# Optimization experiments

Measured on AMD Instinct MI355X. Metric: run time of the kernel, lower is better.

The kernel has to match this reference:

```python
import jax, jax.numpy as jnp
import numpy as np

B, C, D, H, W = 2, 256, 16, 16, 16
R, G = 8, 4  # low rank r=min(8,C//4)=8, groups g=min(4,C)=4
N = D * H * W


def setup_inputs() -> dict:
    key = jax.random.key(0)
    ks = jax.random.split(key, 16)
    s = 0.05  # weight scale keeps softmax logits in a sane range
    inp = {
        'fL': jax.random.normal(ks[0], (B, C, D, H, W), jnp.float32),
        'fU': jax.random.normal(ks[1], (B, C, D, H, W), jnp.float32),
        'qL_w': jax.random.normal(ks[2], (R, C), jnp.float32) * s,
        'qL_b': jnp.zeros((R,), jnp.float32),
        'kU_w': jax.random.normal(ks[3], (R, C), jnp.float32) * s,
        'kU_b': jnp.zeros((R,), jnp.float32),
        'vU_w': jax.random.normal(ks[4], (G, C // G, C // G), jnp.float32) * s,
        'vU_b': jnp.zeros((C,), jnp.float32),
        'qU_w': jax.random.normal(ks[5], (R, C), jnp.float32) * s,
        'qU_b': jnp.zeros((R,), jnp.float32),
        'kL_w': jax.random.normal(ks[6], (R, C), jnp.float32) * s,
        'kL_b': jnp.zeros((R,), jnp.float32),
        'vL_w': jax.random.normal(ks[7], (G, C // G, C // G), jnp.float32) * s,
        'vL_b': jnp.zeros((C,), jnp.float32),
        'beta': jnp.float32(0.5),
    }
    return inp


def _conv1x1(x, w, b):
    # x: [B, C, N]; w: [O, C] (1x1x1 conv == per-voxel linear)
    return jnp.einsum('oc,bcn->bon', w, x) + b[None, :, None]


def _gconv1x1(x, w, b):
    # grouped 1x1x1 conv; x: [B, C, N]; w: [G, Cg_out, Cg_in]
    xg = x.reshape(B, G, C // G, N)
    yg = jnp.einsum('goi,bgin->bgon', w, xg)
    return yg.reshape(B, C, N) + b[None, :, None]


def _attend(q, k, v):
    # q,k: [B, R, N]; v: [B, C, N]
    attn = jax.nn.softmax(jnp.einsum('brn,brm->bnm', q, k), axis=-1)  # [B,N,N]
    return jnp.einsum('bcn,bnm->bcm', v, attn)  # bmm(v, attn)


def reference(fL, fU, qL_w, qL_b, kU_w, kU_b, vU_w, vU_b,
              qU_w, qU_b, kL_w, kL_b, vL_w, vL_b, beta):
    xL = fL.reshape(B, C, N)
    xU = fU.reshape(B, C, N)
    LU = _attend(_conv1x1(xL, qL_w, qL_b), _conv1x1(xU, kU_w, kU_b),
                 _gconv1x1(xU, vU_w, vU_b))
    UL = _attend(_conv1x1(xU, qU_w, qU_b), _conv1x1(xL, kL_w, kL_b),
                 _gconv1x1(xL, vL_w, vL_b))
    fL2 = fL + beta * LU.reshape(B, C, D, H, W)
    fU2 = fU + beta * UL.reshape(B, C, D, H, W)
    return (fL2, fU2)
```

## Files before the change

kernel.cpp:

```cpp
#include <hip/hip_runtime.h>
#include <hip/hip_bf16.h>

#define B_  2
#define C_  256
#define N_  4096
#define R_  8
#define G_  4
#define CG_ 64

typedef __attribute__((ext_vector_type(8))) short short8;
typedef __attribute__((ext_vector_type(4))) float f32x4;

#define MFMA16(a, b, c) __builtin_amdgcn_mfma_f32_16x16x32_bf16((a), (b), (c), 0, 0, 0)
#define EXP2F(x) __builtin_amdgcn_exp2f(x)
#define LOG2E 1.44269504088896f

__device__ inline unsigned int pk2(float a, float b) {
    union { __hip_bfloat162 h; unsigned int u; } cv;
    cv.h = __float22bfloat162_rn(float2{a, b});
    return cv.u;
}
__device__ inline unsigned short f2bf(float f) {
    union { __hip_bfloat16 h; unsigned short u; } cv;
    cv.h = __float2bfloat16(f);
    return cv.u;
}

#define QF_OFF   0
#define KF_OFF   524288
#define VF_OFF   1048576
#define L2Z_OFFF 2621440

#define XS2 264

__global__ __launch_bounds__(256) void fused_pre(
    const float* __restrict__ fL, const float* __restrict__ fU,
    const float* __restrict__ qLw, const float* __restrict__ qLb,
    const float* __restrict__ kLw, const float* __restrict__ kLb,
    const float* __restrict__ vLw, const float* __restrict__ vLb,
    const float* __restrict__ qUw, const float* __restrict__ qUb,
    const float* __restrict__ kUw, const float* __restrict__ kUb,
    const float* __restrict__ vUw, const float* __restrict__ vUb,
    unsigned short* __restrict__ wsu)
{
    const int s   = blockIdx.z >> 1;
    const int b   = blockIdx.z & 1;
    const int nc0 = blockIdx.x;
    const int n0  = nc0 * 32;
    const int t   = threadIdx.x;

    const float* x  = (s ? fU : fL) + (size_t)b * C_ * N_;
    const float* wq = s ? qUw : qLw;
    const float* bq = s ? qUb : qLb;
    const float* wk = s ? kUw : kLw;
    const float* bk = s ? kUb : kLb;
    const float* wv = s ? vUw : vLw;
    const float* bv = s ? vUb : vLb;
    const int dq = s, dk = 1 - s, dv = 1 - s;

    __shared__ __align__(16) unsigned short xs[32 * XS2];
    __shared__ __align__(16) unsigned short vtmp[256 * 48];
    __shared__ __align__(16) float qtmp[2][16][17];

    {
        const int cp = t >> 1;
        const int nh = (t & 1) * 16;
        const float* r0 = x + (size_t)(2 * cp) * N_ + n0 + nh;
        const float* r1 = r0 + N_;
        float4 a[4], bb[4];
#pragma unroll
        for (int j = 0; j < 4; j++) {
            a[j]  = *reinterpret_cast<const float4*>(r0 + j * 4);
            bb[j] = *reinterpret_cast<const float4*>(r1 + j * 4);
        }
        unsigned int* xd = reinterpret_cast<unsigned int*>(xs);
#pragma unroll
        for (int j = 0; j < 4; j++) {
            xd[(nh + j * 4 + 0) * (XS2 / 2) + cp] = pk2(a[j].x, bb[j].x);
            xd[(nh + j * 4 + 1) * (XS2 / 2) + cp] = pk2(a[j].y, bb[j].y);
            xd[(nh + j * 4 + 2) * (XS2 / 2) + cp] = pk2(a[j].z, bb[j].z);
            xd[(nh + j * 4 + 3) * (XS2 / 2) + cp] = pk2(a[j].w, bb[j].w);
        }
    }
    __syncthreads();

    const int w  = t >> 6;
    const int l  = t & 63;
    const int lm = l & 15;
    const int q  = l >> 4;
    const int ncl = w & 1;
    const int gh  = w >> 1;

    short8 bf[8];
    const unsigned short* xrow = xs + (ncl * 16 + lm) * XS2 + q * 8;
    if (gh == 0) {
#pragma unroll
        for (int kc = 0; kc < 8; kc++)
            bf[kc] = *reinterpret_cast<const short8*>(xrow + kc * 32);
    } else {
#pragma unroll
        for (int kc = 4; kc < 8; kc++)
            bf[kc] = *reinterpret_cast<const short8*>(xrow + kc * 32);
    }

    if (gh == 0) {
        const int o = lm;
        const float* wrow = (o < 8) ? (wq + o * C_) : (wk + (o - 8) * C_);
        const float scl = (o < 8) ? LOG2E : 1.0f;
        f32x4 pa = {0.f, 0.f, 0.f, 0.f};
#pragma unroll
        for (int kc = 0; kc < 8; kc++) {
            const float4 w0 = *reinterpret_cast<const float4*>(wrow + kc * 32 + q * 8);
            const float4 w1 = *reinterpret_cast<const float4*>(wrow + kc * 32 + q * 8 + 4);
            union { unsigned int u[4]; short8 v; } aw;
            aw.u[0] = pk2(w0.x * scl, w0.y * scl);
            aw.u[1] = pk2(w0.z * scl, w0.w * scl);
            aw.u[2] = pk2(w1.x * scl, w1.y * scl);
            aw.u[3] = pk2(w1.z * scl, w1.w * scl);
            pa = MFMA16(aw.v, bf[kc], pa);
        }
#pragma unroll
        for (int r = 0; r < 4; r++) {
            const int oo = q * 4 + r;
            const float v = pa[r] + ((q < 2) ? bq[oo] * LOG2E : bk[oo - 8]);
            qtmp[w][oo][lm] = v;
        }
        const int nt = nc0 * 2 + w;
        uint4 pq = {0u, 0u, 0u, 0u}, pk = {0u, 0u, 0u, 0u};
        if (q == 0) {
            float aq[8], ak[8];
#pragma unroll
            for (int o2 = 0; o2 < 8; o2++) { aq[o2] = qtmp[w][o2][lm]; ak[o2] = qtmp[w][8 + o2][lm]; }
            pq.x = pk2(aq[0], aq[1]); pq.y = pk2(aq[2], aq[3]);
            pq.z = pk2(aq[4], aq[5]); pq.w = pk2(aq[6], aq[7]);
            pk.x = pk2(ak[0], ak[1]); pk.y = pk2(ak[2], ak[3]);
            pk.z = pk2(ak[4], ak[5]); pk.w = pk2(ak[6], ak[7]);
        }
        *reinterpret_cast<uint4*>(wsu + QF_OFF + ((size_t)(dq * B_ + b) * 256 + nt) * 512 + l * 8) = pq;
        *reinterpret_cast<uint4*>(wsu + KF_OFF + ((size_t)(dk * B_ + b) * 256 + nt) * 512 + l * 8) = pk;
    }

    {
#pragma unroll
        for (int gi = 0; gi < 2; gi++) {
            const int g = gh * 2 + gi;
#pragma unroll
            for (int ocb = 0; ocb < 4; ocb++) {
                f32x4 ca = {0.f, 0.f, 0.f, 0.f};
#pragma unroll
                for (int kc2 = 0; kc2 < 2; kc2++) {
                    const float* wr = wv + (size_t)g * (CG_ * CG_)
                                    + (ocb * 16 + lm) * CG_ + kc2 * 32 + q * 8;
                    const float4 w0 = *reinterpret_cast<const float4*>(wr);
                    const float4 w1 = *reinterpret_cast<const float4*>(wr + 4);
                    union { unsigned int u[4]; short8 v; } aw;
                    aw.u[0] = pk2(w0.x, w0.y); aw.u[1] = pk2(w0.z, w0.w);
                    aw.u[2] = pk2(w1.x, w1.y); aw.u[3] = pk2(w1.z, w1.w);
                    ca = MFMA16(aw.v, bf[g * 2 + kc2], ca);
                }
#pragma unroll
                for (int r = 0; r < 4; r++) {
                    const int c = g * 64 + ocb * 16 + q * 4 + r;
                    vtmp[c * 48 + ncl * 16 + lm] = f2bf(ca[r] + bv[c]);
                }
            }
        }
    }
    __syncthreads();

    {
        const int db = dv * B_ + b;
#pragma unroll
        for (int ctl = 0; ctl < 4; ctl++) {
            const int ct = w * 4 + ctl;
            const uint4 v4 = *reinterpret_cast<const uint4*>(vtmp + (ct * 16 + lm) * 48 + q * 8);
            *reinterpret_cast<uint4*>(
                wsu + VF_OFF + ((size_t)(db * 16 + ct) * 128 + nc0) * 512 + l * 8) = v4;
        }
    }
}

__global__ __launch_bounds__(256) void zcalc(const unsigned short* __restrict__ wsu,
                                             float* __restrict__ wsf)
{
    const int d   = blockIdx.z;
    const int b   = blockIdx.y;
    const int nc0 = blockIdx.x;
    const int db  = d * B_ + b;
    const int t   = threadIdx.x;
    const int w   = t >> 6;
    const int l   = t & 63;
    const int lm  = l & 15;
    const int q   = l >> 4;

    const unsigned short* qF = wsu + QF_OFF + (size_t)db * 256 * 512;
    const unsigned short* kF = wsu + KF_OFF + (size_t)db * 256 * 512;

    const short8 qf0 = *reinterpret_cast<const short8*>(qF + (size_t)(nc0 * 2 + 0) * 512 + l * 8);
    const short8 qf1 = *reinterpret_cast<const short8*>(qF + (size_t)(nc0 * 2 + 1) * 512 + l * 8);

    const f32x4 zero = {0.f, 0.f, 0.f, 0.f};
    float za0[4] = {0.f, 0.f, 0.f, 0.f};
    float za1[4] = {0.f, 0.f, 0.f, 0.f};

    short8 kc_ = *reinterpret_cast<const short8*>(kF + (size_t)(w * 64) * 512 + l * 8);
    for (int it = 0; it < 64; it++) {
        const int nmt = w * 64 + ((it + 1) & 63);
        const short8 kn = *reinterpret_cast<const short8*>(kF + (size_t)nmt * 512 + l * 8);
        const f32x4 s0 = MFMA16(qf0, kc_, zero);
        const f32x4 s1 = MFMA16(qf1, kc_, zero);
#pragma unroll
        for (int r = 0; r < 4; r++) { za0[r] += EXP2F(s0[r]); za1[r] += EXP2F(s1[r]); }
        kc_ = kn;
    }

#pragma unroll
    for (int r = 0; r < 4; r++) {
        za0[r] += __shfl_xor(za0[r], 1); za0[r] += __shfl_xor(za0[r], 2);
        za0[r] += __shfl_xor(za0[r], 4); za0[r] += __shfl_xor(za0[r], 8);
        za1[r] += __shfl_xor(za1[r], 1); za1[r] += __shfl_xor(za1[r], 2);
        za1[r] += __shfl_xor(za1[r], 4); za1[r] += __shfl_xor(za1[r], 8);
    }

    __shared__ __align__(16) float zred[4][2][16];
    if (lm == 0) {
        *reinterpret_cast<float4*>(&zred[w][0][q * 4]) = float4{za0[0], za0[1], za0[2], za0[3]};
        *reinterpret_cast<float4*>(&zred[w][1][q * 4]) = float4{za1[0], za1[1], za1[2], za1[3]};
    }
    __syncthreads();
    if (t < 32) {
        const float Z = zred[0][t >> 4][t & 15] + zred[1][t >> 4][t & 15]
                      + zred[2][t >> 4][t & 15] + zred[3][t >> 4][t & 15];
        wsf[L2Z_OFFF + (size_t)db * N_ + nc0 * 32 + t] = -__log2f(Z);
    }
}

#define ESTR 72

__global__ __launch_bounds__(256) void attn_gemm(
    const float* __restrict__ fL, const float* __restrict__ fU,
    const float* __restrict__ betap,
    const unsigned short* __restrict__ wsu,
    const float* __restrict__ wsf,
    float* __restrict__ out)
{
    const int db = blockIdx.z;
    const int d  = db >> 1;
    const int b  = db & 1;
    const int t  = threadIdx.x;
    const int w  = t >> 6;
    const int l  = t & 63;
    const int lm = l & 15;
    const int q  = l >> 4;
    const int m0 = blockIdx.x * 32;

    const unsigned short* qF = wsu + QF_OFF + (size_t)db * 256 * 512;
    const unsigned short* kF = wsu + KF_OFF + (size_t)db * 256 * 512;
    const unsigned short* VF = wsu + VF_OFF + (size_t)db * 16 * 128 * 512;
    const float* l2z = wsf + L2Z_OFFF + (size_t)db * N_;
    const float* f = ((d == 0) ? fL : fU) + (size_t)b * C_ * N_;
    float*       o = out + (size_t)db * C_ * N_;

    __shared__ __align__(16) unsigned short Es[2][32 * ESTR];

    short8 kf[2];
#pragma unroll
    for (int mb = 0; mb < 2; mb++)
        kf[mb] = *reinterpret_cast<const short8*>(
            kF + (size_t)(blockIdx.x * 2 + mb) * 512 + l * 8);

    const unsigned short* Ab[4];
#pragma unroll
    for (int cb = 0; cb < 4; cb++)
        Ab[cb] = VF + (size_t)(w * 4 + cb) * 128 * 512 + l * 8;

    f32x4 acc[4][2];
#pragma unroll
    for (int cb = 0; cb < 4; cb++)
#pragma unroll
        for (int mb = 0; mb < 2; mb++) acc[cb][mb] = f32x4{0.f, 0.f, 0.f, 0.f};

    short8 A0[8], A1[8], q0, q1;
    f32x4  z0, z1;

    auto loadA = [&](short8* A, int i) {
        const int nc = (i & 63) * 2;
#pragma unroll
        for (int cb = 0; cb < 4; cb++)
#pragma unroll
            for (int kc = 0; kc < 2; kc++)
                A[cb * 2 + kc] = *reinterpret_cast<const short8*>(
                    Ab[cb] + (size_t)(nc + kc) * 512);
    };
    auto loadQZ = [&](short8& qf_, f32x4& zf_, int i) {
        const int ii = i & 63;
        qf_ = *reinterpret_cast<const short8*>(qF + (size_t)(ii * 4 + w) * 512 + l * 8);
        zf_ = *reinterpret_cast<const f32x4*>(l2z + ii * 64 + w * 16 + q * 4);
    };
    auto egen = [&](const short8& qf_, const f32x4& zf_, unsigned short* Eb) {
#pragma unroll
        for (int mb = 0; mb < 2; mb++) {
            const f32x4 sv = MFMA16(qf_, kf[mb], zf_);
            uint2 p;
            p.x = pk2(EXP2F(sv[0]), EXP2F(sv[1]));
            p.y = pk2(EXP2F(sv[2]), EXP2F(sv[3]));
            *reinterpret_cast<uint2*>(Eb + (mb * 16 + lm) * ESTR + w * 16 + q * 4) = p;
        }
    };
    auto mainm = [&](const short8* A, const unsigned short* Eb) {
        short8 Bf[2][2];
#pragma unroll
        for (int mb = 0; mb < 2; mb++)
#pragma unroll
            for (int kc = 0; kc < 2; kc++)
                Bf[mb][kc] = *reinterpret_cast<const short8*>(
                    Eb + (mb * 16 + lm) * ESTR + kc * 32 + q * 8);
#pragma unroll
        for (int kc = 0; kc < 2; kc++)
#pragma unroll
            for (int cb = 0; cb < 4; cb++)
#pragma unroll
                for (int mb = 0; mb < 2; mb++)
                    acc[cb][mb] = MFMA16(A[cb * 2 + kc], Bf[mb][kc], acc[cb][mb]);
    };

    loadA(A0, 0);
    loadQZ(q0, z0, 0);

    for (int i = 0; i < 64; i += 2) {
        egen(q0, z0, Es[0]);
        __syncthreads();
        loadA(A1, i + 1); loadQZ(q1, z1, i + 1);
        mainm(A0, Es[0]);

        egen(q1, z1, Es[1]);
        __syncthreads();
        loadA(A0, i + 2); loadQZ(q0, z0, i + 2);
        mainm(A1, Es[1]);
    }

    const float beta = *betap;
#pragma unroll
    for (int cb = 0; cb < 4; cb++) {
#pragma unroll
        for (int mb = 0; mb < 2; mb++) {
            const int c = w * 64 + cb * 16 + q * 4;
            const int m = m0 + mb * 16 + lm;
#pragma unroll
            for (int r = 0; r < 4; r++) {
                const size_t off = (size_t)(c + r) * N_ + m;
                o[off] = f[off] + beta * acc[cb][mb][r];
            }
        }
    }
}

extern "C" void kernel_launch(void* const* d_in, const int* in_sizes, int n_in,
                              void* d_out, int out_size, void* d_ws, size_t ws_size,
                              hipStream_t stream)
{
    const float* fL   = (const float*)d_in[0];
    const float* fU   = (const float*)d_in[1];
    const float* qL_w = (const float*)d_in[2];
    const float* qL_b = (const float*)d_in[3];
    const float* kU_w = (const float*)d_in[4];
    const float* kU_b = (const float*)d_in[5];
    const float* vU_w = (const float*)d_in[6];
    const float* vU_b = (const float*)d_in[7];
    const float* qU_w = (const float*)d_in[8];
    const float* qU_b = (const float*)d_in[9];
    const float* kL_w = (const float*)d_in[10];
    const float* kL_b = (const float*)d_in[11];
    const float* vL_w = (const float*)d_in[12];
    const float* vL_b = (const float*)d_in[13];
    const float* beta = (const float*)d_in[14];

    unsigned short* wsu  = (unsigned short*)d_ws;
    float*          wsf  = (float*)d_ws;
    float*          outf = (float*)d_out;

    fused_pre<<<dim3(128, 1, 4), 256, 0, stream>>>(
        fL, fU, qL_w, qL_b, kL_w, kL_b, vL_w, vL_b,
        qU_w, qU_b, kU_w, kU_b, vU_w, vU_b, wsu);

    zcalc<<<dim3(128, B_, 2), 256, 0, stream>>>(wsu, wsf);

    attn_gemm<<<dim3(128, 1, 4), 256, 0, stream>>>(
        fL, fU, beta, wsu, wsf, outf);
}
```

Before: 191.3 us.

## Prepack weights to bf16 fragments and retile attention GEMM with XCD-aware grid

Adds a small kernel that converts the q/k/v weights once into bf16 MFMA fragment layout, so fused_pre no longer converts fp32 weights in every block. It also loads x as fp32 into shared memory with coalesced rows before converting, instead of packing pairs of channels. The attention GEMM now uses 64-column m-tiles split across two channel halves, with a flat grid whose block index is mapped so each (direction, batch, channel-half) combination lands on one XCD for L2 locality. The trade-off is an extra kernel launch plus a changed workspace layout, and each block now generates a larger E tile per iteration.

```diff
diff --git a/kernel.cpp b/kernel.cpp
--- a/kernel.cpp
+++ b/kernel.cpp
@@ -29,18 +29,45 @@
 #define QF_OFF   0
 #define KF_OFF   524288
 #define VF_OFF   1048576
-#define L2Z_OFFF 2621440
-
-#define XS2 264
+#define WQKF_OFF 5242880
+#define WVF_OFF  5251072
+#define L2Z_OFFF 2641920
+
+__global__ __launch_bounds__(256) void wpack(
+    const float* __restrict__ qLw, const float* __restrict__ kLw,
+    const float* __restrict__ vLw,
+    const float* __restrict__ qUw, const float* __restrict__ kUw,
+    const float* __restrict__ vUw,
+    unsigned short* __restrict__ wsu)
+{
+    const int s = blockIdx.x;
+    const float* wq = s ? qUw : qLw;
+    const float* wk = s ? kUw : kLw;
+    const float* wv = s ? vUw : vLw;
+
+    for (int i = threadIdx.x; i < 8 * 512; i += 256) {
+        const int kc = i >> 9, l = (i >> 3) & 63, j = i & 7;
+        const int o = l & 15, c = kc * 32 + (l >> 4) * 8 + j;
+        const float v = (o < 8) ? wq[o * C_ + c] * LOG2E : wk[(o - 8) * C_ + c];
+        wsu[WQKF_OFF + s * 4096 + i] = f2bf(v);
+    }
+    for (int i = threadIdx.x; i < 16384; i += 256) {
+        const int g = i >> 12, r1 = i & 4095;
+        const int ocb = r1 >> 10, r2 = r1 & 1023;
+        const int kc2 = r2 >> 9, l = (r2 >> 3) & 63, j = r2 & 7;
+        const int oc = ocb * 16 + (l & 15), ic = kc2 * 32 + (l >> 4) * 8 + j;
+        wsu[WVF_OFF + s * 16384 + i] = f2bf(wv[g * (CG_ * CG_) + oc * CG_ + ic]);
+    }
+}
+
+#define XSTR 260
 
 __global__ __launch_bounds__(256) void fused_pre(
     const float* __restrict__ fL, const float* __restrict__ fU,
-    const float* __restrict__ qLw, const float* __restrict__ qLb,
-    const float* __restrict__ kLw, const float* __restrict__ kLb,
-    const float* __restrict__ vLw, const float* __restrict__ vLb,
-    const float* __restrict__ qUw, const float* __restrict__ qUb,
-    const float* __restrict__ kUw, const float* __restrict__ kUb,
-    const float* __restrict__ vUw, const float* __restrict__ vUb,
+    const float* __restrict__ qLb, const float* __restrict__ kLb,
+    const float* __restrict__ vLb,
+    const float* __restrict__ qUb, const float* __restrict__ kUb,
+    const float* __restrict__ vUb,
     unsigned short* __restrict__ wsu)
 {
     const int s   = blockIdx.z >> 1;
@@ -50,80 +77,72 @@
     const int t   = threadIdx.x;
 
     const float* x  = (s ? fU : fL) + (size_t)b * C_ * N_;
-    const float* wq = s ? qUw : qLw;
     const float* bq = s ? qUb : qLb;
-    const float* wk = s ? kUw : kLw;
     const float* bk = s ? kUb : kLb;
-    const float* wv = s ? vUw : vLw;
     const float* bv = s ? vUb : vLb;
     const int dq = s, dk = 1 - s, dv = 1 - s;
 
-    __shared__ __align__(16) unsigned short xs[32 * XS2];
+    __shared__ __align__(16) float xsf[32 * XSTR];
     __shared__ __align__(16) unsigned short vtmp[256 * 48];
     __shared__ __align__(16) float qtmp[2][16][17];
-
-    {
-        const int cp = t >> 1;
-        const int nh = (t & 1) * 16;
-        const float* r0 = x + (size_t)(2 * cp) * N_ + n0 + nh;
-        const float* r1 = r0 + N_;
-        float4 a[4], bb[4];
-#pragma unroll
-        for (int j = 0; j < 4; j++) {
-            a[j]  = *reinterpret_cast<const float4*>(r0 + j * 4);
-            bb[j] = *reinterpret_cast<const float4*>(r1 + j * 4);
-        }
-        unsigned int* xd = reinterpret_cast<unsigned int*>(xs);
-#pragma unroll
-        for (int j = 0; j < 4; j++) {
-            xd[(nh + j * 4 + 0) * (XS2 / 2) + cp] = pk2(a[j].x, bb[j].x);
-            xd[(nh + j * 4 + 1) * (XS2 / 2) + cp] = pk2(a[j].y, bb[j].y);
-            xd[(nh + j * 4 + 2) * (XS2 / 2) + cp] = pk2(a[j].z, bb[j].z);
-            xd[(nh + j * 4 + 3) * (XS2 / 2) + cp] = pk2(a[j].w, bb[j].w);
-        }
-    }
-    __syncthreads();
 
     const int w  = t >> 6;
     const int l  = t & 63;
     const int lm = l & 15;
     const int q  = l >> 4;
+
+    {
+        const int cr  = w * 8 + (l >> 3);
+        const int ncl_ = (l & 7) * 4;
+        float4 xv[8];
+#pragma unroll
+        for (int it = 0; it < 8; it++)
+            xv[it] = *reinterpret_cast<const float4*>(
+                x + (size_t)(it * 32 + cr) * N_ + n0 + ncl_);
+#pragma unroll
+        for (int it = 0; it < 8; it++) {
+            const int c = it * 32 + cr;
+            xsf[(ncl_ + 0) * XSTR + c] = xv[it].x;
+            xsf[(ncl_ + 1) * XSTR + c] = xv[it].y;
+            xsf[(ncl_ + 2) * XSTR + c] = xv[it].z;
+            xsf[(ncl_ + 3) * XSTR + c] = xv[it].w;
+        }
+    }
+    __syncthreads();
+
     const int ncl = w & 1;
     const int gh  = w >> 1;
+    const int nrow = ncl * 16 + lm;
+    const int n = n0 + nrow;
 
     short8 bf[8];
-    const unsigned short* xrow = xs + (ncl * 16 + lm) * XS2 + q * 8;
+    {
+        const float* xr = xsf + nrow * XSTR + q * 8;
+        const int kclo = (gh == 0) ? 0 : 4;
+#pragma unroll
+        for (int kc = 0; kc < 8; kc++) {
+            if (kc < kclo) continue;
+            const float4 f0 = *reinterpret_cast<const float4*>(xr + kc * 32);
+            const float4 f1 = *reinterpret_cast<const float4*>(xr + kc * 32 + 4);
+            union { unsigned int u[4]; short8 v; } bb;
+            bb.u[0] = pk2(f0.x, f0.y); bb.u[1] = pk2(f0.z, f0.w);
+            bb.u[2] = pk2(f1.x, f1.y); bb.u[3] = pk2(f1.z, f1.w);
+            bf[kc] = bb.v;
+        }
+    }
+
     if (gh == 0) {
-#pragma unroll
-        for (int kc = 0; kc < 8; kc++)
-            bf[kc] = *reinterpret_cast<const short8*>(xrow + kc * 32);
-    } else {
-#pragma unroll
-        for (int kc = 4; kc < 8; kc++)
-            bf[kc] = *reinterpret_cast<const short8*>(xrow + kc * 32);
-    }
-
-    if (gh == 0) {
-        const int o = lm;
-        const float* wrow = (o < 8) ? (wq + o * C_) : (wk + (o - 8) * C_);
-        const float scl = (o < 8) ? LOG2E : 1.0f;
+        const unsigned short* wb = wsu + WQKF_OFF + s * 4096;
         f32x4 pa = {0.f, 0.f, 0.f, 0.f};
 #pragma unroll
         for (int kc = 0; kc < 8; kc++) {
-            const float4 w0 = *reinterpret_cast<const float4*>(wrow + kc * 32 + q * 8);
-            const float4 w1 = *reinterpret_cast<const float4*>(wrow + kc * 32 + q * 8 + 4);
-            union { unsigned int u[4]; short8 v; } aw;
-            aw.u[0] = pk2(w0.x * scl, w0.y * scl);
-            aw.u[1] = pk2(w0.z * scl, w0.w * scl);
-            aw.u[2] = pk2(w1.x * scl, w1.y * scl);
-            aw.u[3] = pk2(w1.z * scl, w1.w * scl);
-            pa = MFMA16(aw.v, bf[kc], pa);
+            const short8 af = *reinterpret_cast<const short8*>(wb + kc * 512 + l * 8);
+            pa = MFMA16(af, bf[kc], pa);
         }
 #pragma unroll
         for (int r = 0; r < 4; r++) {
             const int oo = q * 4 + r;
-            const float v = pa[r] + ((q < 2) ? bq[oo] * LOG2E : bk[oo - 8]);
-            qtmp[w][oo][lm] = v;
+            qtmp[w][oo][lm] = pa[r] + ((q < 2) ? bq[oo] * LOG2E : bk[oo - 8]);
         }
         const int nt = nc0 * 2 + w;
         uint4 pq = {0u, 0u, 0u, 0u}, pk = {0u, 0u, 0u, 0u};
@@ -141,6 +160,7 @@
     }
 
     {
+        const unsigned short* vb = wsu + WVF_OFF + s * 16384;
 #pragma unroll
         for (int gi = 0; gi < 2; gi++) {
             const int g = gh * 2 + gi;
@@ -149,14 +169,9 @@
                 f32x4 ca = {0.f, 0.f, 0.f, 0.f};
 #pragma unroll
                 for (int kc2 = 0; kc2 < 2; kc2++) {
-                    const float* wr = wv + (size_t)g * (CG_ * CG_)
-                                    + (ocb * 16 + lm) * CG_ + kc2 * 32 + q * 8;
-                    const float4 w0 = *reinterpret_cast<const float4*>(wr);
-                    const float4 w1 = *reinterpret_cast<const float4*>(wr + 4);
-                    union { unsigned int u[4]; short8 v; } aw;
-                    aw.u[0] = pk2(w0.x, w0.y); aw.u[1] = pk2(w0.z, w0.w);
-                    aw.u[2] = pk2(w1.x, w1.y); aw.u[3] = pk2(w1.z, w1.w);
-                    ca = MFMA16(aw.v, bf[g * 2 + kc2], ca);
+                    const short8 af = *reinterpret_cast<const short8*>(
+                        vb + (((g * 4 + ocb) * 2 + kc2) * 512) + l * 8);
+                    ca = MFMA16(af, bf[g * 2 + kc2], ca);
                 }
 #pragma unroll
                 for (int r = 0; r < 4; r++) {
@@ -244,7 +259,11 @@
     const float* __restrict__ wsf,
     float* __restrict__ out)
 {
-    const int db = blockIdx.z;
+    const int id = blockIdx.x;
+    const int xcd = id & 7;
+    const int db = xcd >> 1;
+    const int ch = xcd & 1;
+    const int mt = id >> 3;
     const int d  = db >> 1;
     const int b  = db & 1;
     const int t  = threadIdx.x;
@@ -252,7 +271,9 @@
     const int l  = t & 63;
     const int lm = l & 15;
     const int q  = l >> 4;
-    const int m0 = blockIdx.x * 32;
+    const int wc = w & 1;
+    const int wm = w >> 1;
+    const int m0 = mt * 64;
 
     const unsigned short* qF = wsu + QF_OFF + (size_t)db * 256 * 512;
     const unsigned short* kF = wsu + KF_OFF + (size_t)db * 256 * 512;
@@ -261,18 +282,18 @@
     const float* f = ((d == 0) ? fL : fU) + (size_t)b * C_ * N_;
     float*       o = out + (size_t)db * C_ * N_;
 
-    __shared__ __align__(16) unsigned short Es[2][32 * ESTR];
+    __shared__ __align__(16) unsigned short Es[2][64 * ESTR];
 
     short8 kf[2];
 #pragma unroll
     for (int mb = 0; mb < 2; mb++)
         kf[mb] = *reinterpret_cast<const short8*>(
-            kF + (size_t)(blockIdx.x * 2 + mb) * 512 + l * 8);
+            kF + (size_t)(mt * 4 + wm * 2 + mb) * 512 + l * 8);
 
     const unsigned short* Ab[4];
 #pragma unroll
     for (int cb = 0; cb < 4; cb++)
-        Ab[cb] = VF + (size_t)(w * 4 + cb) * 128 * 512 + l * 8;
+        Ab[cb] = VF + (size_t)(ch * 8 + wc * 4 + cb) * 128 * 512 + l * 8;
 
     f32x4 acc[4][2];
 #pragma unroll
@@ -280,8 +301,8 @@
 #pragma unroll
         for (int mb = 0; mb < 2; mb++) acc[cb][mb] = f32x4{0.f, 0.f, 0.f, 0.f};
 
-    short8 A0[8], A1[8], q0, q1;
-    f32x4  z0, z1;
+    short8 A0[8], A1[8], q0[2], q1[2];
+    f32x4  z0[2], z1[2];
 
     auto loadA = [&](short8* A, int i) {
         const int nc = (i & 63) * 2;
@@ -292,20 +313,28 @@
                 A[cb * 2 + kc] = *reinterpret_cast<const short8*>(
                     Ab[cb] + (size_t)(nc + kc) * 512);
     };
-    auto loadQZ = [&](short8& qf_, f32x4& zf_, int i) {
+    auto loadQZ = [&](short8* qA, f32x4* zf, int i) {
         const int ii = i & 63;
-        qf_ = *reinterpret_cast<const short8*>(qF + (size_t)(ii * 4 + w) * 512 + l * 8);
-        zf_ = *reinterpret_cast<const f32x4*>(l2z + ii * 64 + w * 16 + q * 4);
+#pragma unroll
+        for (int nc = 0; nc < 2; nc++) {
+            qA[nc] = *reinterpret_cast<const short8*>(
+                qF + (size_t)(ii * 4 + wc * 2 + nc) * 512 + l * 8);
+            zf[nc] = *reinterpret_cast<const f32x4*>(
+                l2z + ii * 64 + wc * 32 + nc * 16 + q * 4);
+        }
     };
-    auto egen = [&](const short8& qf_, const f32x4& zf_, unsigned short* Eb) {
-#pragma unroll
-        for (int mb = 0; mb < 2; mb++) {
-            const f32x4 sv = MFMA16(qf_, kf[mb], zf_);
-            uint2 p;
-            p.x = pk2(EXP2F(sv[0]), EXP2F(sv[1]));
-            p.y = pk2(EXP2F(sv[2]), EXP2F(sv[3]));
-            *reinterpret_cast<uint2*>(Eb + (mb * 16 + lm) * ESTR + w * 16 + q * 4) = p;
-        }
+    auto egen = [&](const short8* qA, const f32x4* zf, unsigned short* Eb) {
+#pragma unroll
+        for (int mb = 0; mb < 2; mb++)
+#pragma unroll
+            for (int nc = 0; nc < 2; nc++) {
+                const f32x4 sv = MFMA16(qA[nc], kf[mb], zf[nc]);
+                uint2 p;
+                p.x = pk2(EXP2F(sv[0]), EXP2F(sv[1]));
+                p.y = pk2(EXP2F(sv[2]), EXP2F(sv[3]));
+                *reinterpret_cast<uint2*>(
+                    Eb + (wm * 32 + mb * 16 + lm) * ESTR + wc * 32 + nc * 16 + q * 4) = p;
+            }
     };
     auto mainm = [&](const short8* A, const unsigned short* Eb) {
         short8 Bf[2][2];
@@ -314,7 +343,7 @@
 #pragma unroll
             for (int kc = 0; kc < 2; kc++)
                 Bf[mb][kc] = *reinterpret_cast<const short8*>(
-                    Eb + (mb * 16 + lm) * ESTR + kc * 32 + q * 8);
+                    Eb + (wm * 32 + mb * 16 + lm) * ESTR + kc * 32 + q * 8);
 #pragma unroll
         for (int kc = 0; kc < 2; kc++)
 #pragma unroll
@@ -344,8 +373,8 @@
     for (int cb = 0; cb < 4; cb++) {
 #pragma unroll
         for (int mb = 0; mb < 2; mb++) {
-            const int c = w * 64 + cb * 16 + q * 4;
-            const int m = m0 + mb * 16 + lm;
+            const int c = ch * 128 + wc * 64 + cb * 16 + q * 4;
+            const int m = m0 + wm * 32 + mb * 16 + lm;
 #pragma unroll
             for (int r = 0; r < 4; r++) {
                 const size_t off = (size_t)(c + r) * N_ + m;
@@ -379,12 +408,13 @@
     float*          wsf  = (float*)d_ws;
     float*          outf = (float*)d_out;
 
+    wpack<<<dim3(2), 256, 0, stream>>>(qL_w, kL_w, vL_w, qU_w, kU_w, vU_w, wsu);
+
     fused_pre<<<dim3(128, 1, 4), 256, 0, stream>>>(
-        fL, fU, qL_w, qL_b, kL_w, kL_b, vL_w, vL_b,
-        qU_w, qU_b, kU_w, kU_b, vU_w, vU_b, wsu);
+        fL, fU, qL_b, kL_b, vL_b, qU_b, kU_b, vU_b, wsu);
 
     zcalc<<<dim3(128, B_, 2), 256, 0, stream>>>(wsu, wsf);
 
-    attn_gemm<<<dim3(128, 1, 4), 256, 0, stream>>>(
+    attn_gemm<<<dim3(512), 256, 0, stream>>>(
         fL, fU, beta, wsu, wsf, outf);
 }
```

New measurement: 218.8 us. 14.4% more time.

## Double K-step per iteration in attn_gemm and stage fp32 input in LDS

Applied to the files above, without the earlier changes.

The attention GEMM now processes 128 keys per iteration instead of 64, halving the number of barriers and generating twice as many exp tiles per step. The A-fragment loads move to a single buffer issued after the MFMAs, replacing the double-buffered registers. The preprocessing kernel now stages fp32 input in shared memory with coalesced row loads and converts to bf16 at fragment-read time, and LDS strides are padded differently. This trades more LDS and register pressure, plus less overlap of the A loads, for fewer synchronizations.

```diff
diff --git a/kernel.cpp b/kernel.cpp
--- a/kernel.cpp
+++ b/kernel.cpp
@@ -31,7 +31,8 @@
 #define VF_OFF   1048576
 #define L2Z_OFFF 2621440
 
-#define XS2 264
+#define XSTR 260
+#define VTS  56
 
 __global__ __launch_bounds__(256) void fused_pre(
     const float* __restrict__ fL, const float* __restrict__ fU,
@@ -58,49 +59,53 @@
     const float* bv = s ? vUb : vLb;
     const int dq = s, dk = 1 - s, dv = 1 - s;
 
-    __shared__ __align__(16) unsigned short xs[32 * XS2];
-    __shared__ __align__(16) unsigned short vtmp[256 * 48];
+    __shared__ __align__(16) float xsf[32 * XSTR];
+    __shared__ __align__(16) unsigned short vtmp[256 * VTS];
     __shared__ __align__(16) float qtmp[2][16][17];
-
-    {
-        const int cp = t >> 1;
-        const int nh = (t & 1) * 16;
-        const float* r0 = x + (size_t)(2 * cp) * N_ + n0 + nh;
-        const float* r1 = r0 + N_;
-        float4 a[4], bb[4];
-#pragma unroll
-        for (int j = 0; j < 4; j++) {
-            a[j]  = *reinterpret_cast<const float4*>(r0 + j * 4);
-            bb[j] = *reinterpret_cast<const float4*>(r1 + j * 4);
-        }
-        unsigned int* xd = reinterpret_cast<unsigned int*>(xs);
-#pragma unroll
-        for (int j = 0; j < 4; j++) {
-            xd[(nh + j * 4 + 0) * (XS2 / 2) + cp] = pk2(a[j].x, bb[j].x);
-            xd[(nh + j * 4 + 1) * (XS2 / 2) + cp] = pk2(a[j].y, bb[j].y);
-            xd[(nh + j * 4 + 2) * (XS2 / 2) + cp] = pk2(a[j].z, bb[j].z);
-            xd[(nh + j * 4 + 3) * (XS2 / 2) + cp] = pk2(a[j].w, bb[j].w);
-        }
-    }
-    __syncthreads();
 
     const int w  = t >> 6;
     const int l  = t & 63;
     const int lm = l & 15;
     const int q  = l >> 4;
+
+    {
+        const int cr   = w * 8 + (l >> 3);
+        const int ncl_ = (l & 7) * 4;
+        float4 xv[8];
+#pragma unroll
+        for (int it = 0; it < 8; it++)
+            xv[it] = *reinterpret_cast<const float4*>(
+                x + (size_t)(it * 32 + cr) * N_ + n0 + ncl_);
+#pragma unroll
+        for (int it = 0; it < 8; it++) {
+            const int c = it * 32 + cr;
+            xsf[(ncl_ + 0) * XSTR + c] = xv[it].x;
+            xsf[(ncl_ + 1) * XSTR + c] = xv[it].y;
+            xsf[(ncl_ + 2) * XSTR + c] = xv[it].z;
+            xsf[(ncl_ + 3) * XSTR + c] = xv[it].w;
+        }
+    }
+    __syncthreads();
+
     const int ncl = w & 1;
     const int gh  = w >> 1;
+    const int nrow = ncl * 16 + lm;
+    const int n = n0 + nrow;
 
     short8 bf[8];
-    const unsigned short* xrow = xs + (ncl * 16 + lm) * XS2 + q * 8;
-    if (gh == 0) {
-#pragma unroll
-        for (int kc = 0; kc < 8; kc++)
-            bf[kc] = *reinterpret_cast<const short8*>(xrow + kc * 32);
-    } else {
-#pragma unroll
-        for (int kc = 4; kc < 8; kc++)
-            bf[kc] = *reinterpret_cast<const short8*>(xrow + kc * 32);
+    {
+        const float* xr = xsf + nrow * XSTR + q * 8;
+        const int kclo = (gh == 0) ? 0 : 4;
+#pragma unroll
+        for (int kc = 0; kc < 8; kc++) {
+            if (kc < kclo) continue;
+            const float4 f0 = *reinterpret_cast<const float4*>(xr + kc * 32);
+            const float4 f1 = *reinterpret_cast<const float4*>(xr + kc * 32 + 4);
+            union { unsigned int u[4]; short8 v; } bb;
+            bb.u[0] = pk2(f0.x, f0.y); bb.u[1] = pk2(f0.z, f0.w);
+            bb.u[2] = pk2(f1.x, f1.y); bb.u[3] = pk2(f1.z, f1.w);
+            bf[kc] = bb.v;
+        }
     }
 
     if (gh == 0) {
@@ -122,8 +127,7 @@
 #pragma unroll
         for (int r = 0; r < 4; r++) {
             const int oo = q * 4 + r;
-            const float v = pa[r] + ((q < 2) ? bq[oo] * LOG2E : bk[oo - 8]);
-            qtmp[w][oo][lm] = v;
+            qtmp[w][oo][lm] = pa[r] + ((q < 2) ? bq[oo] * LOG2E : bk[oo - 8]);
         }
         const int nt = nc0 * 2 + w;
         uint4 pq = {0u, 0u, 0u, 0u}, pk = {0u, 0u, 0u, 0u};
@@ -161,7 +165,7 @@
 #pragma unroll
                 for (int r = 0; r < 4; r++) {
                     const int c = g * 64 + ocb * 16 + q * 4 + r;
-                    vtmp[c * 48 + ncl * 16 + lm] = f2bf(ca[r] + bv[c]);
+                    vtmp[c * VTS + ncl * 16 + lm] = f2bf(ca[r] + bv[c]);
                 }
             }
         }
@@ -173,7 +177,7 @@
 #pragma unroll
         for (int ctl = 0; ctl < 4; ctl++) {
             const int ct = w * 4 + ctl;
-            const uint4 v4 = *reinterpret_cast<const uint4*>(vtmp + (ct * 16 + lm) * 48 + q * 8);
+            const uint4 v4 = *reinterpret_cast<const uint4*>(vtmp + (ct * 16 + lm) * VTS + q * 8);
             *reinterpret_cast<uint4*>(
                 wsu + VF_OFF + ((size_t)(db * 16 + ct) * 128 + nc0) * 512 + l * 8) = v4;
         }
@@ -235,7 +239,7 @@
     }
 }
 
-#define ESTR 72
+#define ESTR 136
 
 __global__ __launch_bounds__(256) void attn_gemm(
     const float* __restrict__ fL, const float* __restrict__ fU,
@@ -280,63 +284,74 @@
 #pragma unroll
         for (int mb = 0; mb < 2; mb++) acc[cb][mb] = f32x4{0.f, 0.f, 0.f, 0.f};
 
-    short8 A0[8], A1[8], q0, q1;
-    f32x4  z0, z1;
-
-    auto loadA = [&](short8* A, int i) {
-        const int nc = (i & 63) * 2;
+    short8 A[16];
+    short8 q0[2], q1[2];
+    f32x4  z0[2], z1[2];
+
+    auto loadA = [&](int i) {
+        const int nc = (i & 31) * 4;
 #pragma unroll
         for (int cb = 0; cb < 4; cb++)
 #pragma unroll
-            for (int kc = 0; kc < 2; kc++)
-                A[cb * 2 + kc] = *reinterpret_cast<const short8*>(
+            for (int kc = 0; kc < 4; kc++)
+                A[cb * 4 + kc] = *reinterpret_cast<const short8*>(
                     Ab[cb] + (size_t)(nc + kc) * 512);
     };
-    auto loadQZ = [&](short8& qf_, f32x4& zf_, int i) {
-        const int ii = i & 63;
-        qf_ = *reinterpret_cast<const short8*>(qF + (size_t)(ii * 4 + w) * 512 + l * 8);
-        zf_ = *reinterpret_cast<const f32x4*>(l2z + ii * 64 + w * 16 + q * 4);
+    auto loadQZ = [&](short8* qA, f32x4* zf, int i) {
+        const int ii = i & 31;
+#pragma unroll
+        for (int nc = 0; nc < 2; nc++) {
+            qA[nc] = *reinterpret_cast<const short8*>(
+                qF + (size_t)(ii * 8 + w * 2 + nc) * 512 + l * 8);
+            zf[nc] = *reinterpret_cast<const f32x4*>(
+                l2z + ii * 128 + w * 32 + nc * 16 + q * 4);
+        }
     };
-    auto egen = [&](const short8& qf_, const f32x4& zf_, unsigned short* Eb) {
-#pragma unroll
-        for (int mb = 0; mb < 2; mb++) {
-            const f32x4 sv = MFMA16(qf_, kf[mb], zf_);
-            uint2 p;
-            p.x = pk2(EXP2F(sv[0]), EXP2F(sv[1]));
-            p.y = pk2(EXP2F(sv[2]), EXP2F(sv[3]));
-            *reinterpret_cast<uint2*>(Eb + (mb * 16 + lm) * ESTR + w * 16 + q * 4) = p;
-        }
+    auto egen = [&](const short8* qA, const f32x4* zf, unsigned short* Eb) {
+#pragma unroll
+        for (int mb = 0; mb < 2; mb++)
+#pragma unroll
+            for (int nc = 0; nc < 2; nc++) {
+                const f32x4 sv = MFMA16(qA[nc], kf[mb], zf[nc]);
+                uint2 p;
+                p.x = pk2(EXP2F(sv[0]), EXP2F(sv[1]));
+                p.y = pk2(EXP2F(sv[2]), EXP2F(sv[3]));
+                *reinterpret_cast<uint2*>(
+                    Eb + (mb * 16 + lm) * ESTR + w * 32 + nc * 16 + q * 4) = p;
+            }
     };
-    auto mainm = [&](const short8* A, const unsigned short* Eb) {
-        short8 Bf[2][2];
-#pragma unroll
-        for (int mb = 0; mb < 2; mb++)
-#pragma unroll
-            for (int kc = 0; kc < 2; kc++)
-                Bf[mb][kc] = *reinterpret_cast<const short8*>(
+    auto mainm = [&](const unsigned short* Eb) {
+#pragma unroll
+        for (int kc = 0; kc < 4; kc++) {
+            short8 Bf[2];
+#pragma unroll
+            for (int mb = 0; mb < 2; mb++)
+                Bf[mb] = *reinterpret_cast<const short8*>(
                     Eb + (mb * 16 + lm) * ESTR + kc * 32 + q * 8);
 #pragma unroll
-        for (int kc = 0; kc < 2; kc++)
-#pragma unroll
             for (int cb = 0; cb < 4; cb++)
 #pragma unroll
                 for (int mb = 0; mb < 2; mb++)
-                    acc[cb][mb] = MFMA16(A[cb * 2 + kc], Bf[mb][kc], acc[cb][mb]);
+                    acc[cb][mb] = MFMA16(A[cb * 4 + kc], Bf[mb], acc[cb][mb]);
+        }
     };
 
-    loadA(A0, 0);
     loadQZ(q0, z0, 0);
-
-    for (int i = 0; i < 64; i += 2) {
+    loadA(0);
+    loadQZ(q1, z1, 1);
+
+    for (int i = 0; i < 32; i += 2) {
         egen(q0, z0, Es[0]);
         __syncthreads();
-        loadA(A1, i + 1); loadQZ(q1, z1, i + 1);
-        mainm(A0, Es[0]);
+        loadQZ(q0, z0, i + 2);
+        mainm(Es[0]);
+        loadA(i + 1);
 
         egen(q1, z1, Es[1]);
         __syncthreads();
-        loadA(A0, i + 2); loadQZ(q0, z0, i + 2);
-        mainm(A1, Es[1]);
+        loadQZ(q1, z1, i + 3);
+        mainm(Es[1]);
+        loadA(i + 2);
     }
 
     const float beta = *betap;
```

Measured after the change: 185.5 us. 1.03x faster.
